# Performance work log

Hardware: AMD Instinct MI355X
Metric: run time of the kernel (lower is better)

Reference implementation:

```python
import jax, jax.numpy as jnp
import numpy as np

B, N, D, S = 16, 128, 128, 128   # batch, n_nodes, node/edge feat dim, state_dim
MP_INT = 256
UP_INT = 256
EPS = 1e-3  # keras BatchNormalization default epsilon


def _mlp(x, W1, b1, W2, b2):
    # Dense(relu) -> Dense(relu)
    h = jax.nn.relu(x @ W1 + b1)
    return jax.nn.relu(h @ W2 + b2)


def setup_inputs() -> dict:
    key = jax.random.key(0)
    ks = jax.random.split(key, 16)
    g = lambda k, shape: jax.random.normal(k, shape, dtype=jnp.float32) * 0.05
    nodes = jax.random.normal(ks[0], (B, N, D), dtype=jnp.float32)
    edges = jax.random.normal(ks[1], (B, N * N, D), dtype=jnp.float32)
    mask = (jax.random.uniform(ks[2], (B, N * N, 1)) > 0.5).astype(jnp.float32)
    return {
        "nodes": nodes, "edges": edges, "mask": mask,
        # Adj_Updater_1: concat(node_i, node_j, edge_ij) -> UP_INT -> S
        "W1a": g(ks[3], (3 * D, UP_INT)), "b1a": jnp.zeros((UP_INT,), jnp.float32),
        "W2a": g(ks[4], (UP_INT, S)), "b2a": jnp.zeros((S,), jnp.float32),
        # Message_Passer_1: concat(node_i, node_j, new_edge) -> MP_INT -> S
        "W1m": g(ks[5], (2 * D + S, MP_INT)), "b1m": jnp.zeros((MP_INT,), jnp.float32),
        "W2m": g(ks[6], (MP_INT, S)), "b2m": jnp.zeros((S,), jnp.float32),
        # Update_Func_1: concat(old_state, agg_messages) -> UP_INT -> S
        "W1u": g(ks[7], (D + S, UP_INT)), "b1u": jnp.zeros((UP_INT,), jnp.float32),
        "W2u": g(ks[8], (UP_INT, S)), "b2u": jnp.zeros((S,), jnp.float32),
        # BatchNorm (inference mode: moving stats) for nodes and edges
        "gamma_n": jnp.ones((S,), jnp.float32), "beta_n": jnp.zeros((S,), jnp.float32),
        "mean_n": jnp.zeros((S,), jnp.float32), "var_n": jnp.ones((S,), jnp.float32),
        "gamma_e": jnp.ones((S,), jnp.float32), "beta_e": jnp.zeros((S,), jnp.float32),
        "mean_e": jnp.zeros((S,), jnp.float32), "var_e": jnp.ones((S,), jnp.float32),
    }


def reference(nodes, edges, mask,
              W1a, b1a, W2a, b2a,
              W1m, b1m, W2m, b2m,
              W1u, b1u, W2u, b2u,
              gamma_n, beta_n, mean_n, var_n,
              gamma_e, beta_e, mean_e, var_e):
    b, n, d = nodes.shape
    # tf.tile(nodes,[1,n,1]): row p*n+q -> nodes[q]  (state_i)
    state_i = jnp.broadcast_to(nodes[:, None, :, :], (b, n, n, d)).reshape(b, n * n, d)
    # reshape(tile(nodes,[1,1,n])): row p*n+q -> nodes[p]  (state_j)
    state_j = jnp.broadcast_to(nodes[:, :, None, :], (b, n, n, d)).reshape(b, n * n, d)

    new_edges = _mlp(jnp.concatenate([state_i, state_j, edges], axis=-1), W1a, b1a, W2a, b2a)
    new_edges = new_edges * mask

    messages = _mlp(jnp.concatenate([state_i, state_j, new_edges], axis=-1), W1m, b1m, W2m, b2m)
    masked = (messages * mask).reshape(b, n, n, -1)
    agg_m = masked.sum(axis=2)  # reduce over axis 2 as in Message_Agg

    state_1 = _mlp(jnp.concatenate([nodes, agg_m], axis=-1), W1u, b1u, W2u, b2u)

    bn = lambda x, g_, b_, m_, v_: g_ * (x - m_) * jax.lax.rsqrt(v_ + EPS) + b_
    nodes_out = bn(state_1, gamma_n, beta_n, mean_n, var_n)
    edges_out = bn(new_edges, gamma_e, beta_e, mean_e, var_e)
    return nodes_out, edges_out
```

## Files before the change

kernel.cpp:

```cpp
#include <hip/hip_runtime.h>
#include <hip/hip_bf16.h>
#include <cstdint>
#include <cstddef>


typedef __attribute__((ext_vector_type(8))) __bf16 bf16x8;
typedef __attribute__((ext_vector_type(4))) float f32x4;

#define GLDS(gp, lp)                                                        \
  __builtin_amdgcn_global_load_lds(                                         \
      (const __attribute__((address_space(1))) void*)(gp),                  \
      (__attribute__((address_space(3))) void*)(lp), 16, 0, 0)

__device__ inline bf16x8 load8_cvt(const float* __restrict__ p) {
  const float4 a = *(const float4*)p;
  const float4 b = *(const float4*)(p + 4);
  bf16x8 r;
  r[0] = (__bf16)a.x; r[1] = (__bf16)a.y; r[2] = (__bf16)a.z; r[3] = (__bf16)a.w;
  r[4] = (__bf16)b.x; r[5] = (__bf16)b.y; r[6] = (__bf16)b.z; r[7] = (__bf16)b.w;
  return r;
}

__global__ void __launch_bounds__(256) proj_kernel(
    const float* __restrict__ nodes, const float* __restrict__ W1a,
    const float* __restrict__ b1a, const float* __restrict__ W1m,
    const float* __restrict__ b1m, float* __restrict__ outP) {
  __shared__ float x[8][128];
  const int mat = blockIdx.y;
  const int t = threadIdx.x;
  const float* W = (mat < 2 ? W1a : W1m) + ((mat & 1) ? 128 * 256 : 0);
  float* out = outP + (size_t)mat * (2048 * 256);
  const int r0 = blockIdx.x * 8;
  for (int i = t; i < 1024; i += 256)
    x[i >> 7][i & 127] = nodes[r0 * 128 + i];
  __syncthreads();
  float bv = 0.f;
  if (mat == 1) bv = b1a[t];
  if (mat == 3) bv = b1m[t];
  float acc[8];
#pragma unroll
  for (int r = 0; r < 8; ++r) acc[r] = bv;
  for (int k = 0; k < 128; ++k) {
    float w = W[k * 256 + t];
#pragma unroll
    for (int r = 0; r < 8; ++r) acc[r] += x[r][k] * w;
  }
  for (int r = 0; r < 8; ++r) out[(size_t)(r0 + r) * 256 + t] = acc[r];
}

__global__ void __launch_bounds__(256) wswz_kernel(
    const float* __restrict__ W1a, const float* __restrict__ W2a,
    const float* __restrict__ W1m, const float* __restrict__ W2m,
    __hip_bfloat16* __restrict__ dstp) {
  __bf16* dst = (__bf16*)dstp;
  const int mat = blockIdx.y;
  const float* src;
  __bf16* d;
  int nsh;
  if (mat == 0)      { src = W1a + 65536; d = dst;         nsh = 8; }
  else if (mat == 1) { src = W2a;         d = dst + 32768; nsh = 7; }
  else if (mat == 2) { src = W1m + 65536; d = dst + 65536; nsh = 8; }
  else               { src = W2m;         d = dst + 98304; nsh = 7; }
  const int nmask = (1 << nsh) - 1;
  const int base = (blockIdx.x * 256 + threadIdx.x) * 4;
#pragma unroll
  for (int i = 0; i < 4; ++i) {
    int s = base + i;
    int k = s >> nsh, n = s & nmask;
    float v = src[s];
    int g = k >> 3;
    if (nsh == 8) {
      int gs = (g & 8) | ((g ^ n) & 7);
      d[n * 128 + gs * 8 + (k & 7)] = (__bf16)v;
    } else {
      int gs = (g ^ n) & 7;
      d[((k >> 6) << 13) + (n << 6) + (gs << 3) + (k & 7)] = (__bf16)v;
    }
  }
}

__global__ void __launch_bounds__(256, 2) fused_mlp_kernel(
    const float* __restrict__ edges, const float* __restrict__ mask,
    const float* __restrict__ b2a, const float* __restrict__ b2m,
    const float* __restrict__ ge, const float* __restrict__ be,
    const float* __restrict__ me, const float* __restrict__ ve,
    const float* __restrict__ Pa, const float* __restrict__ Qab,
    const float* __restrict__ Pm, const float* __restrict__ Qmb,
    const __hip_bfloat16* __restrict__ Wsw, float* __restrict__ edges_out,
    float* __restrict__ agg) {
  __shared__ __align__(16) char sArena[49152];
  char* const sW1h = sArena;
  char* const sW2h = sArena + 16384;
  char* const sH1q = sArena + 32768;
  float* const sAgg = (float*)(sArena + 32768);
  __shared__ float sQ[256];
  __shared__ float sB2a[128];
  __shared__ float sB2m[128];
  __shared__ float sMask[128];
  __shared__ float sScE[128];
  __shared__ float sShE[128];

  const int t = threadIdx.x;
  const int lane = t & 63, wv = t >> 6;
  const int cl = lane & 15, qd = lane >> 4;
  const int m0 = wv * 32;

  const int sw = ((blockIdx.x & 7) << 6) | (blockIdx.x >> 3);
  const int bb = sw >> 5;
  const int p = sw & 31;
  const int p0 = p * 4;

  if (t < 128) {
    sB2a[t] = b2a[t];
    sB2m[t] = b2m[t];
    float sc = ge[t] * rsqrtf(ve[t] + 1e-3f);
    sScE[t] = sc;
    sShE[t] = be[t] - me[t] * sc;
  }

  const char* gW1e = (const char*)Wsw;
  const char* gW2e = (const char*)(Wsw + 32768);
  const char* gW1m = (const char*)(Wsw + 65536);
  const char* gW2m = (const char*)(Wsw + 98304);

  for (int tp = 0; tp < 4; ++tp) {
    const int pp = p0 + tp;
    __syncthreads();
    sQ[t] = Qab[((bb << 7) + pp) * 256 + t];
    if (t < 128) sMask[t] = mask[(bb << 14) + (pp << 7) + t];

    const float* Xb = edges + ((size_t)((bb << 14) + (pp << 7)) << 7);
    bf16x8 xf[2][4];
#pragma unroll
    for (int mt = 0; mt < 2; ++mt)
#pragma unroll
      for (int ks = 0; ks < 4; ++ks)
        xf[mt][ks] = load8_cvt(Xb + (m0 + mt * 16 + cl) * 128 + ks * 32 + qd * 8);

    f32x4 ne[2][8];
#pragma unroll
    for (int mt = 0; mt < 2; ++mt)
#pragma unroll
      for (int nt = 0; nt < 8; ++nt) {
        float bv = sB2a[nt * 16 + cl];
        ne[mt][nt] = (f32x4){bv, bv, bv, bv};
      }

    for (int h = 0; h < 4; ++h) {
      __syncthreads();
      {
        const char* gW1 = gW1e + h * 16384;
        const char* gW2 = gW2e + h * 16384;
        for (int o = wv * 1024; o < 16384; o += 4096) {
          GLDS(gW1 + o + lane * 16, sW1h + o);
          GLDS(gW2 + o + lane * 16, sW2h + o);
        }
      }
      f32x4 a1[2][4];
#pragma unroll
      for (int mt = 0; mt < 2; ++mt)
#pragma unroll
        for (int nt = 0; nt < 4; ++nt) {
          const int col = h * 64 + nt * 16 + cl;
          const int mrow = m0 + mt * 16 + qd * 4;
          const float qv = sQ[col];
          const float* pa = Pa + (size_t)((bb << 7) + mrow) * 256 + col;
          a1[mt][nt] = (f32x4){pa[0] + qv, pa[256] + qv, pa[512] + qv, pa[768] + qv};
        }
      __syncthreads();
#pragma unroll
      for (int ks = 0; ks < 4; ++ks)
#pragma unroll
        for (int nt = 0; nt < 4; ++nt) {
          const int nl = nt * 16 + cl;
          const int g = ks * 4 + qd;
          const int gs = (g & 8) | ((g ^ nl) & 7);
          bf16x8 bw = *(const bf16x8*)(sW1h + nl * 256 + gs * 16);
          a1[0][nt] = __builtin_amdgcn_mfma_f32_16x16x32_bf16(xf[0][ks], bw, a1[0][nt], 0, 0, 0);
          a1[1][nt] = __builtin_amdgcn_mfma_f32_16x16x32_bf16(xf[1][ks], bw, a1[1][nt], 0, 0, 0);
        }
#pragma unroll
      for (int mt = 0; mt < 2; ++mt)
#pragma unroll
        for (int nt = 0; nt < 4; ++nt) {
          const int kq = nt * 16 + cl;
#pragma unroll
          for (int r = 0; r < 4; ++r) {
            const int m = m0 + mt * 16 + qd * 4 + r;
            float v = a1[mt][nt][r];
            v = v > 0.f ? v : 0.f;
            const int gs = ((kq >> 3) ^ m) & 7;
            *(__bf16*)(sH1q + m * 128 + gs * 16 + (kq & 7) * 2) = (__bf16)v;
          }
        }
      bf16x8 hf[2][2];
#pragma unroll
      for (int mt = 0; mt < 2; ++mt)
#pragma unroll
        for (int ks = 0; ks < 2; ++ks) {
          const int m = m0 + mt * 16 + cl;
          const int g = ks * 4 + qd;
          const int gs = (g ^ m) & 7;
          hf[mt][ks] = *(const bf16x8*)(sH1q + m * 128 + gs * 16);
        }
#pragma unroll
      for (int ks = 0; ks < 2; ++ks)
#pragma unroll
        for (int nt = 0; nt < 8; ++nt) {
          const int n = nt * 16 + cl;
          const int g = ks * 4 + qd;
          const int gs = (g ^ n) & 7;
          bf16x8 bw = *(const bf16x8*)(sW2h + n * 128 + gs * 16);
          ne[0][nt] = __builtin_amdgcn_mfma_f32_16x16x32_bf16(hf[0][ks], bw, ne[0][nt], 0, 0, 0);
          ne[1][nt] = __builtin_amdgcn_mfma_f32_16x16x32_bf16(hf[1][ks], bw, ne[1][nt], 0, 0, 0);
        }
    }

    __syncthreads();
    sQ[t] = Qmb[((bb << 7) + pp) * 256 + t];
    {
      float* Ob = edges_out + ((size_t)((bb << 14) + (pp << 7)) << 7);
#pragma unroll
      for (int mt = 0; mt < 2; ++mt)
#pragma unroll
        for (int nt = 0; nt < 8; ++nt) {
          const int col = nt * 16 + cl;
          const float sc = sScE[col], sh = sShE[col];
          char* const buf = (nt & 4) ? sW2h : sW1h;
          const int kq = col & 63;
#pragma unroll
          for (int r = 0; r < 4; ++r) {
            const int m = m0 + mt * 16 + qd * 4 + r;
            float v = ne[mt][nt][r];
            v = v > 0.f ? v : 0.f;
            const float e = v * sMask[m];
            Ob[m * 128 + col] = e * sc + sh;
            const int gs = ((kq >> 3) ^ m) & 7;
            *(__bf16*)(buf + m * 128 + gs * 16 + (kq & 7) * 2) = (__bf16)e;
          }
        }
    }
    __syncthreads();

    bf16x8 xf2[2][4];
#pragma unroll
    for (int mt = 0; mt < 2; ++mt)
#pragma unroll
      for (int ks = 0; ks < 4; ++ks) {
        const int m = m0 + mt * 16 + cl;
        const int g = (ks & 1) * 4 + qd;
        const int gs = (g ^ m) & 7;
        const char* buf = (ks & 2) ? sW2h : sW1h;
        xf2[mt][ks] = *(const bf16x8*)(buf + m * 128 + gs * 16);
      }

    f32x4 ms[2][8];
#pragma unroll
    for (int mt = 0; mt < 2; ++mt)
#pragma unroll
      for (int nt = 0; nt < 8; ++nt) {
        float bv = sB2m[nt * 16 + cl];
        ms[mt][nt] = (f32x4){bv, bv, bv, bv};
      }

    for (int h = 0; h < 4; ++h) {
      __syncthreads();
      {
        const char* gW1 = gW1m + h * 16384;
        const char* gW2 = gW2m + h * 16384;
        for (int o = wv * 1024; o < 16384; o += 4096) {
          GLDS(gW1 + o + lane * 16, sW1h + o);
          GLDS(gW2 + o + lane * 16, sW2h + o);
        }
      }
      f32x4 a1[2][4];
#pragma unroll
      for (int mt = 0; mt < 2; ++mt)
#pragma unroll
        for (int nt = 0; nt < 4; ++nt) {
          const int col = h * 64 + nt * 16 + cl;
          const int mrow = m0 + mt * 16 + qd * 4;
          const float qv = sQ[col];
          const float* pa = Pm + (size_t)((bb << 7) + mrow) * 256 + col;
          a1[mt][nt] = (f32x4){pa[0] + qv, pa[256] + qv, pa[512] + qv, pa[768] + qv};
        }
      __syncthreads();
#pragma unroll
      for (int ks = 0; ks < 4; ++ks)
#pragma unroll
        for (int nt = 0; nt < 4; ++nt) {
          const int nl = nt * 16 + cl;
          const int g = ks * 4 + qd;
          const int gs = (g & 8) | ((g ^ nl) & 7);
          bf16x8 bw = *(const bf16x8*)(sW1h + nl * 256 + gs * 16);
          a1[0][nt] = __builtin_amdgcn_mfma_f32_16x16x32_bf16(xf2[0][ks], bw, a1[0][nt], 0, 0, 0);
          a1[1][nt] = __builtin_amdgcn_mfma_f32_16x16x32_bf16(xf2[1][ks], bw, a1[1][nt], 0, 0, 0);
        }
#pragma unroll
      for (int mt = 0; mt < 2; ++mt)
#pragma unroll
        for (int nt = 0; nt < 4; ++nt) {
          const int kq = nt * 16 + cl;
#pragma unroll
          for (int r = 0; r < 4; ++r) {
            const int m = m0 + mt * 16 + qd * 4 + r;
            float v = a1[mt][nt][r];
            v = v > 0.f ? v : 0.f;
            const int gs = ((kq >> 3) ^ m) & 7;
            *(__bf16*)(sH1q + m * 128 + gs * 16 + (kq & 7) * 2) = (__bf16)v;
          }
        }
      bf16x8 hf[2][2];
#pragma unroll
      for (int mt = 0; mt < 2; ++mt)
#pragma unroll
        for (int ks = 0; ks < 2; ++ks) {
          const int m = m0 + mt * 16 + cl;
          const int g = ks * 4 + qd;
          const int gs = (g ^ m) & 7;
          hf[mt][ks] = *(const bf16x8*)(sH1q + m * 128 + gs * 16);
        }
#pragma unroll
      for (int ks = 0; ks < 2; ++ks)
#pragma unroll
        for (int nt = 0; nt < 8; ++nt) {
          const int n = nt * 16 + cl;
          const int g = ks * 4 + qd;
          const int gs = (g ^ n) & 7;
          bf16x8 bw = *(const bf16x8*)(sW2h + n * 128 + gs * 16);
          ms[0][nt] = __builtin_amdgcn_mfma_f32_16x16x32_bf16(hf[0][ks], bw, ms[0][nt], 0, 0, 0);
          ms[1][nt] = __builtin_amdgcn_mfma_f32_16x16x32_bf16(hf[1][ks], bw, ms[1][nt], 0, 0, 0);
        }
    }

    float ss[8];
#pragma unroll
    for (int nt = 0; nt < 8; ++nt) {
      float s = 0.f;
#pragma unroll
      for (int mt = 0; mt < 2; ++mt)
#pragma unroll
        for (int r = 0; r < 4; ++r) {
          const int m = m0 + mt * 16 + qd * 4 + r;
          float v = ms[mt][nt][r];
          v = v > 0.f ? v : 0.f;
          s += v * sMask[m];
        }
      s += __shfl_xor(s, 16);
      s += __shfl_xor(s, 32);
      ss[nt] = s;
    }
    __syncthreads();
    if (lane < 16) {
#pragma unroll
      for (int nt = 0; nt < 8; ++nt) sAgg[wv * 128 + nt * 16 + lane] = ss[nt];
    }
    __syncthreads();
    if (t < 128)
      agg[((bb << 7) + pp) * 128 + t] =
          sAgg[t] + sAgg[128 + t] + sAgg[256 + t] + sAgg[384 + t];
  }
}

__global__ void __launch_bounds__(256) update_kernel(
    const float* __restrict__ nodes, const float* __restrict__ agg,
    const float* __restrict__ W1u, const float* __restrict__ b1u,
    const float* __restrict__ W2u, const float* __restrict__ b2u,
    const float* __restrict__ gn, const float* __restrict__ btn,
    const float* __restrict__ mn, const float* __restrict__ vn,
    float* __restrict__ out) {
  __shared__ float x[4][256];
  __shared__ float hh[4][256];
  const int t = threadIdx.x;
  const int r0 = blockIdx.x * 4;
  for (int i = t; i < 1024; i += 256) {
    int r = i >> 8, c = i & 255;
    x[r][c] = (c < 128) ? nodes[(r0 + r) * 128 + c] : agg[(r0 + r) * 128 + (c - 128)];
  }
  __syncthreads();
  float acc[4];
  {
    float bv = b1u[t];
#pragma unroll
    for (int r = 0; r < 4; ++r) acc[r] = bv;
  }
  for (int k = 0; k < 256; ++k) {
    float w = W1u[k * 256 + t];
#pragma unroll
    for (int r = 0; r < 4; ++r) acc[r] += x[r][k] * w;
  }
#pragma unroll
  for (int r = 0; r < 4; ++r) hh[r][t] = acc[r] > 0.f ? acc[r] : 0.f;
  __syncthreads();
  const int j = t & 127, half = t >> 7;
  float a2[2];
  {
    float bv = b2u[j];
#pragma unroll
    for (int r = 0; r < 2; ++r) a2[r] = bv;
  }
  for (int k = 0; k < 256; ++k) {
    float w = W2u[k * 128 + j];
#pragma unroll
    for (int r = 0; r < 2; ++r) a2[r] += hh[half * 2 + r][k] * w;
  }
  float sc = gn[j] * rsqrtf(vn[j] + 1e-3f);
  float sh = btn[j] - mn[j] * sc;
#pragma unroll
  for (int r = 0; r < 2; ++r) {
    float v = a2[r] > 0.f ? a2[r] : 0.f;
    out[(r0 + half * 2 + r) * 128 + j] = v * sc + sh;
  }
}

extern "C" void kernel_launch(void* const* d_in, const int* in_sizes, int n_in,
                              void* d_out, int out_size, void* d_ws,
                              size_t ws_size, hipStream_t stream) {
  (void)in_sizes; (void)n_in; (void)out_size; (void)ws_size;
  const float* nodes = (const float*)d_in[0];
  const float* edges = (const float*)d_in[1];
  const float* mask = (const float*)d_in[2];
  const float* W1a = (const float*)d_in[3];
  const float* b1a = (const float*)d_in[4];
  const float* W2a = (const float*)d_in[5];
  const float* b2a = (const float*)d_in[6];
  const float* W1m = (const float*)d_in[7];
  const float* b1m = (const float*)d_in[8];
  const float* W2m = (const float*)d_in[9];
  const float* b2m = (const float*)d_in[10];
  const float* W1u = (const float*)d_in[11];
  const float* b1u = (const float*)d_in[12];
  const float* W2u = (const float*)d_in[13];
  const float* b2u = (const float*)d_in[14];
  const float* gn = (const float*)d_in[15];
  const float* btn = (const float*)d_in[16];
  const float* mn = (const float*)d_in[17];
  const float* vn = (const float*)d_in[18];
  const float* ge = (const float*)d_in[19];
  const float* be = (const float*)d_in[20];
  const float* me = (const float*)d_in[21];
  const float* ve = (const float*)d_in[22];

  float* out_nodes = (float*)d_out;
  float* out_edges = (float*)d_out + 262144;

  char* ws = (char*)d_ws;
  float* Pa = (float*)(ws);
  float* Qab = (float*)(ws + ((size_t)1 << 21));
  float* Pm = (float*)(ws + ((size_t)2 << 21));
  float* Qmb = (float*)(ws + ((size_t)3 << 21));
  float* agg = (float*)(ws + ((size_t)4 << 21));
  __hip_bfloat16* Wsw = (__hip_bfloat16*)(ws + ((size_t)4 << 21) + ((size_t)1 << 20));

  proj_kernel<<<dim3(256, 4), 256, 0, stream>>>(nodes, W1a, b1a, W1m, b1m, Pa);
  wswz_kernel<<<dim3(32, 4), 256, 0, stream>>>(W1a, W2a, W1m, W2m, Wsw);
  fused_mlp_kernel<<<512, 256, 0, stream>>>(edges, mask, b2a, b2m, ge, be, me,
                                            ve, Pa, Qab, Pm, Qmb, Wsw,
                                            out_edges, agg);
  update_kernel<<<512, 256, 0, stream>>>(nodes, agg, W1u, b1u, W2u, b2u, gn, btn,
                                         mn, vn, out_nodes);
}
```

Before: 457.1 us.

## Double-buffer W1 tiles in LDS and transpose P projections for vector loads

The W1 weight slice for the next hidden chunk is now prefetched into a second LDS buffer while the current chunk's MFMAs run, which removes one barrier per chunk and overlaps global-to-LDS staging with compute. The per-node projections Pa/Pm are stored transposed (column-major per batch), so each thread reads four consecutive rows with one float4 load instead of four strided scalar loads. LDS use grows from 48 KB to 64 KB per block, which may limit the two-blocks-per-CU occupancy target. Buffer reuse for the edge-output staging has to stay consistent with the in-flight prefetch.

```diff
diff --git a/kernel.cpp b/kernel.cpp
--- a/kernel.cpp
+++ b/kernel.cpp
@@ -11,6 +11,10 @@
   __builtin_amdgcn_global_load_lds(                                         \
       (const __attribute__((address_space(1))) void*)(gp),                  \
       (__attribute__((address_space(3))) void*)(lp), 16, 0, 0)
+
+#define STAGE16(gsrc, ldst)                                                 \
+  for (int o = wv * 1024; o < 16384; o += 4096)                             \
+    GLDS((gsrc) + o + lane * 16, (ldst) + o);
 
 __device__ inline bf16x8 load8_cvt(const float* __restrict__ p) {
   const float4 a = *(const float4*)p;
@@ -45,7 +49,14 @@
 #pragma unroll
     for (int r = 0; r < 8; ++r) acc[r] += x[r][k] * w;
   }
-  for (int r = 0; r < 8; ++r) out[(size_t)(r0 + r) * 256 + t] = acc[r];
+  if (mat == 0 || mat == 2) {
+    const int bb = r0 >> 7, q0 = r0 & 127;
+    float* o = out + ((size_t)((bb << 8) + t) << 7) + q0;
+#pragma unroll
+    for (int r = 0; r < 8; ++r) o[r] = acc[r];
+  } else {
+    for (int r = 0; r < 8; ++r) out[(size_t)(r0 + r) * 256 + t] = acc[r];
+  }
 }
 
 __global__ void __launch_bounds__(256) wswz_kernel(
@@ -84,15 +95,14 @@
     const float* __restrict__ b2a, const float* __restrict__ b2m,
     const float* __restrict__ ge, const float* __restrict__ be,
     const float* __restrict__ me, const float* __restrict__ ve,
-    const float* __restrict__ Pa, const float* __restrict__ Qab,
-    const float* __restrict__ Pm, const float* __restrict__ Qmb,
+    const float* __restrict__ PaT, const float* __restrict__ Qab,
+    const float* __restrict__ PmT, const float* __restrict__ Qmb,
     const __hip_bfloat16* __restrict__ Wsw, float* __restrict__ edges_out,
     float* __restrict__ agg) {
-  __shared__ __align__(16) char sArena[49152];
-  char* const sW1h = sArena;
-  char* const sW2h = sArena + 16384;
-  char* const sH1q = sArena + 32768;
-  float* const sAgg = (float*)(sArena + 32768);
+  __shared__ __align__(16) char sW1[2][16384];
+  __shared__ __align__(16) char sW2[16384];
+  __shared__ __align__(16) char sH1q[16384];
+  float* const sAgg = (float*)sH1q;
   __shared__ float sQ[256];
   __shared__ float sB2a[128];
   __shared__ float sB2m[128];
@@ -107,8 +117,7 @@
 
   const int sw = ((blockIdx.x & 7) << 6) | (blockIdx.x >> 3);
   const int bb = sw >> 5;
-  const int p = sw & 31;
-  const int p0 = p * 4;
+  const int p0 = (sw & 31) * 4;
 
   if (t < 128) {
     sB2a[t] = b2a[t];
@@ -122,12 +131,15 @@
   const char* gW2e = (const char*)(Wsw + 32768);
   const char* gW1m = (const char*)(Wsw + 65536);
   const char* gW2m = (const char*)(Wsw + 98304);
+  const float* PaTb = PaT + ((size_t)bb << 15);
+  const float* PmTb = PmT + ((size_t)bb << 15);
 
   for (int tp = 0; tp < 4; ++tp) {
     const int pp = p0 + tp;
     __syncthreads();
     sQ[t] = Qab[((bb << 7) + pp) * 256 + t];
     if (t < 128) sMask[t] = mask[(bb << 14) + (pp << 7) + t];
+    STAGE16(gW1e, sW1[0]);
 
     const float* Xb = edges + ((size_t)((bb << 14) + (pp << 7)) << 7);
     bf16x8 xf[2][4];
@@ -146,28 +158,23 @@
         ne[mt][nt] = (f32x4){bv, bv, bv, bv};
       }
 
+#pragma unroll
     for (int h = 0; h < 4; ++h) {
       __syncthreads();
-      {
-        const char* gW1 = gW1e + h * 16384;
-        const char* gW2 = gW2e + h * 16384;
-        for (int o = wv * 1024; o < 16384; o += 4096) {
-          GLDS(gW1 + o + lane * 16, sW1h + o);
-          GLDS(gW2 + o + lane * 16, sW2h + o);
-        }
-      }
+      STAGE16(gW2e + h * 16384, sW2);
+      if (h < 3) { STAGE16(gW1e + (h + 1) * 16384, sW1[(h + 1) & 1]); }
+      else       { STAGE16(gW1m, sW1[0]); }
       f32x4 a1[2][4];
 #pragma unroll
       for (int mt = 0; mt < 2; ++mt)
 #pragma unroll
         for (int nt = 0; nt < 4; ++nt) {
           const int col = h * 64 + nt * 16 + cl;
-          const int mrow = m0 + mt * 16 + qd * 4;
           const float qv = sQ[col];
-          const float* pa = Pa + (size_t)((bb << 7) + mrow) * 256 + col;
-          a1[mt][nt] = (f32x4){pa[0] + qv, pa[256] + qv, pa[512] + qv, pa[768] + qv};
-        }
-      __syncthreads();
+          const float4 pa = *(const float4*)&PaTb[((size_t)col << 7) + m0 +
+                                                  mt * 16 + qd * 4];
+          a1[mt][nt] = (f32x4){pa.x + qv, pa.y + qv, pa.z + qv, pa.w + qv};
+        }
 #pragma unroll
       for (int ks = 0; ks < 4; ++ks)
 #pragma unroll
@@ -175,10 +182,11 @@
           const int nl = nt * 16 + cl;
           const int g = ks * 4 + qd;
           const int gs = (g & 8) | ((g ^ nl) & 7);
-          bf16x8 bw = *(const bf16x8*)(sW1h + nl * 256 + gs * 16);
+          bf16x8 bw = *(const bf16x8*)(sW1[h & 1] + nl * 256 + gs * 16);
           a1[0][nt] = __builtin_amdgcn_mfma_f32_16x16x32_bf16(xf[0][ks], bw, a1[0][nt], 0, 0, 0);
           a1[1][nt] = __builtin_amdgcn_mfma_f32_16x16x32_bf16(xf[1][ks], bw, a1[1][nt], 0, 0, 0);
         }
+      __syncthreads();
 #pragma unroll
       for (int mt = 0; mt < 2; ++mt)
 #pragma unroll
@@ -199,8 +207,7 @@
 #pragma unroll
         for (int ks = 0; ks < 2; ++ks) {
           const int m = m0 + mt * 16 + cl;
-          const int g = ks * 4 + qd;
-          const int gs = (g ^ m) & 7;
+          const int gs = ((ks * 4 + qd) ^ m) & 7;
           hf[mt][ks] = *(const bf16x8*)(sH1q + m * 128 + gs * 16);
         }
 #pragma unroll
@@ -208,9 +215,8 @@
 #pragma unroll
         for (int nt = 0; nt < 8; ++nt) {
           const int n = nt * 16 + cl;
-          const int g = ks * 4 + qd;
-          const int gs = (g ^ n) & 7;
-          bf16x8 bw = *(const bf16x8*)(sW2h + n * 128 + gs * 16);
+          const int gs = ((ks * 4 + qd) ^ n) & 7;
+          bf16x8 bw = *(const bf16x8*)(sW2 + n * 128 + gs * 16);
           ne[0][nt] = __builtin_amdgcn_mfma_f32_16x16x32_bf16(hf[0][ks], bw, ne[0][nt], 0, 0, 0);
           ne[1][nt] = __builtin_amdgcn_mfma_f32_16x16x32_bf16(hf[1][ks], bw, ne[1][nt], 0, 0, 0);
         }
@@ -226,7 +232,7 @@
         for (int nt = 0; nt < 8; ++nt) {
           const int col = nt * 16 + cl;
           const float sc = sScE[col], sh = sShE[col];
-          char* const buf = (nt & 4) ? sW2h : sW1h;
+          char* const buf = (nt & 4) ? sW2 : sW1[1];
           const int kq = col & 63;
 #pragma unroll
           for (int r = 0; r < 4; ++r) {
@@ -240,17 +246,14 @@
           }
         }
     }
-    __syncthreads();
-
     bf16x8 xf2[2][4];
 #pragma unroll
     for (int mt = 0; mt < 2; ++mt)
 #pragma unroll
       for (int ks = 0; ks < 4; ++ks) {
         const int m = m0 + mt * 16 + cl;
-        const int g = (ks & 1) * 4 + qd;
-        const int gs = (g ^ m) & 7;
-        const char* buf = (ks & 2) ? sW2h : sW1h;
+        const int gs = (((ks & 1) * 4 + qd) ^ m) & 7;
+        const char* buf = (ks & 2) ? sW2 : sW1[1];
         xf2[mt][ks] = *(const bf16x8*)(buf + m * 128 + gs * 16);
       }
 
@@ -263,28 +266,22 @@
         ms[mt][nt] = (f32x4){bv, bv, bv, bv};
       }
 
+#pragma unroll
     for (int h = 0; h < 4; ++h) {
       __syncthreads();
-      {
-        const char* gW1 = gW1m + h * 16384;
-        const char* gW2 = gW2m + h * 16384;
-        for (int o = wv * 1024; o < 16384; o += 4096) {
-          GLDS(gW1 + o + lane * 16, sW1h + o);
-          GLDS(gW2 + o + lane * 16, sW2h + o);
-        }
-      }
+      STAGE16(gW2m + h * 16384, sW2);
+      if (h < 3) { STAGE16(gW1m + (h + 1) * 16384, sW1[(h + 1) & 1]); }
       f32x4 a1[2][4];
 #pragma unroll
       for (int mt = 0; mt < 2; ++mt)
 #pragma unroll
         for (int nt = 0; nt < 4; ++nt) {
           const int col = h * 64 + nt * 16 + cl;
-          const int mrow = m0 + mt * 16 + qd * 4;
           const float qv = sQ[col];
-          const float* pa = Pm + (size_t)((bb << 7) + mrow) * 256 + col;
-          a1[mt][nt] = (f32x4){pa[0] + qv, pa[256] + qv, pa[512] + qv, pa[768] + qv};
-        }
-      __syncthreads();
+          const float4 pa = *(const float4*)&PmTb[((size_t)col << 7) + m0 +
+                                                  mt * 16 + qd * 4];
+          a1[mt][nt] = (f32x4){pa.x + qv, pa.y + qv, pa.z + qv, pa.w + qv};
+        }
 #pragma unroll
       for (int ks = 0; ks < 4; ++ks)
 #pragma unroll
@@ -292,10 +289,11 @@
           const int nl = nt * 16 + cl;
           const int g = ks * 4 + qd;
           const int gs = (g & 8) | ((g ^ nl) & 7);
-          bf16x8 bw = *(const bf16x8*)(sW1h + nl * 256 + gs * 16);
+          bf16x8 bw = *(const bf16x8*)(sW1[h & 1] + nl * 256 + gs * 16);
           a1[0][nt] = __builtin_amdgcn_mfma_f32_16x16x32_bf16(xf2[0][ks], bw, a1[0][nt], 0, 0, 0);
           a1[1][nt] = __builtin_amdgcn_mfma_f32_16x16x32_bf16(xf2[1][ks], bw, a1[1][nt], 0, 0, 0);
         }
+      __syncthreads();
 #pragma unroll
       for (int mt = 0; mt < 2; ++mt)
 #pragma unroll
@@ -316,8 +314,7 @@
 #pragma unroll
         for (int ks = 0; ks < 2; ++ks) {
           const int m = m0 + mt * 16 + cl;
-          const int g = ks * 4 + qd;
-          const int gs = (g ^ m) & 7;
+          const int gs = ((ks * 4 + qd) ^ m) & 7;
           hf[mt][ks] = *(const bf16x8*)(sH1q + m * 128 + gs * 16);
         }
 #pragma unroll
@@ -325,9 +322,8 @@
 #pragma unroll
         for (int nt = 0; nt < 8; ++nt) {
           const int n = nt * 16 + cl;
-          const int g = ks * 4 + qd;
-          const int gs = (g ^ n) & 7;
-          bf16x8 bw = *(const bf16x8*)(sW2h + n * 128 + gs * 16);
+          const int gs = ((ks * 4 + qd) ^ n) & 7;
+          bf16x8 bw = *(const bf16x8*)(sW2 + n * 128 + gs * 16);
           ms[0][nt] = __builtin_amdgcn_mfma_f32_16x16x32_bf16(hf[0][ks], bw, ms[0][nt], 0, 0, 0);
           ms[1][nt] = __builtin_amdgcn_mfma_f32_16x16x32_bf16(hf[1][ks], bw, ms[1][nt], 0, 0, 0);
         }
@@ -445,17 +441,17 @@
   float* out_edges = (float*)d_out + 262144;
 
   char* ws = (char*)d_ws;
-  float* Pa = (float*)(ws);
+  float* PaT = (float*)(ws);
   float* Qab = (float*)(ws + ((size_t)1 << 21));
-  float* Pm = (float*)(ws + ((size_t)2 << 21));
+  float* PmT = (float*)(ws + ((size_t)2 << 21));
   float* Qmb = (float*)(ws + ((size_t)3 << 21));
   float* agg = (float*)(ws + ((size_t)4 << 21));
   __hip_bfloat16* Wsw = (__hip_bfloat16*)(ws + ((size_t)4 << 21) + ((size_t)1 << 20));
 
-  proj_kernel<<<dim3(256, 4), 256, 0, stream>>>(nodes, W1a, b1a, W1m, b1m, Pa);
+  proj_kernel<<<dim3(256, 4), 256, 0, stream>>>(nodes, W1a, b1a, W1m, b1m, PaT);
   wswz_kernel<<<dim3(32, 4), 256, 0, stream>>>(W1a, W2a, W1m, W2m, Wsw);
   fused_mlp_kernel<<<512, 256, 0, stream>>>(edges, mask, b2a, b2m, ge, be, me,
-                                            ve, Pa, Qab, Pm, Qmb, Wsw,
+                                            ve, PaT, Qab, PmT, Qmb, Wsw,
                                             out_edges, agg);
   update_kernel<<<512, 256, 0, stream>>>(nodes, agg, W1u, b1u, W2u, b2u, gn, btn,
                                          mn, vn, out_nodes);
```

Measured after the change: 662.9 us. 45.0% more time.
